# Kernel tuning notes

Hardware: AMD Instinct MI355X
Metric: run time of the kernel (lower is better)

The kernel has to match this reference:

```python
import jax, jax.numpy as jnp
import numpy as np

B, TQ, TK, D = 8, 2048, 2048, 1024


def setup_inputs() -> dict:
    key = jax.random.key(0)
    ks = jax.random.split(key, 9)
    s = 1.0 / np.sqrt(D)
    return {
        "query": jax.random.normal(ks[0], (B, TQ, D), jnp.float32),
        "keys": jax.random.normal(ks[1], (B, TK, D), jnp.float32),
        "Wq": jax.random.normal(ks[2], (D, D), jnp.float32) * s,
        "bq": jax.random.normal(ks[3], (D,), jnp.float32) * 0.01,
        "Wk": jax.random.normal(ks[4], (D, D), jnp.float32) * s,
        "bk": jax.random.normal(ks[5], (D,), jnp.float32) * 0.01,
        "Wv": jax.random.normal(ks[6], (D, D), jnp.float32) * s,
        "bv": jax.random.normal(ks[7], (D,), jnp.float32) * 0.01,
        "mask": jax.random.randint(ks[8], (B, TQ, TK), 0, 2, jnp.int32),
    }


def reference(query, keys, Wq, bq, Wk, bk, Wv, bv, mask):
    # Projections (torch Linear math; weights stored as [in, out])
    q = query @ Wq + bq            # [B, TQ, D]
    k = keys @ Wk + bk             # [B, TK, D]
    v = keys @ Wv + bv             # proj_values=True -> [B, TK, D]
    scale = 1.0 / jnp.sqrt(jnp.asarray(D, q.dtype))
    scores = jnp.einsum("bqd,bkd->bqk", q, k) * scale  # [B, TQ, TK]
    scores = jnp.where(mask == 0, jnp.asarray(-1e9, scores.dtype), scores)
    alphas = jax.nn.softmax(scores, axis=-1)
    context = jnp.einsum("bqk,bkd->bqd", alphas, v)    # [B, TQ, D]
    return context
```

## Files before the change

### kernel.cpp

```cpp
#include <hip/hip_runtime.h>
#include <hip/hip_bf16.h>

#define BB 8
#define TQn 2048
#define TKn 2048
#define DDn 1024

typedef float f32x4 __attribute__((ext_vector_type(4)));
typedef short bf16x8 __attribute__((ext_vector_type(8)));

__device__ __forceinline__ void async16(const void* g, void* l) {
    __builtin_amdgcn_global_load_lds(
        (const __attribute__((address_space(1))) void*)g,
        (__attribute__((address_space(3))) void*)l, 16, 0, 0);
}

__global__ __launch_bounds__(256) void cast_f32_bf16_k(
    const float* __restrict__ in, __hip_bfloat16* __restrict__ out, size_t n8) {
    size_t i = (size_t)blockIdx.x * blockDim.x + threadIdx.x;
    size_t stride = (size_t)gridDim.x * blockDim.x;
    for (; i < n8; i += stride) {
        const float4* p = (const float4*)in + i * 2;
        float4 a = p[0], b = p[1];
        union { __hip_bfloat16 h[8]; int4 q; } u;
        u.h[0] = __float2bfloat16(a.x); u.h[1] = __float2bfloat16(a.y);
        u.h[2] = __float2bfloat16(a.z); u.h[3] = __float2bfloat16(a.w);
        u.h[4] = __float2bfloat16(b.x); u.h[5] = __float2bfloat16(b.y);
        u.h[6] = __float2bfloat16(b.z); u.h[7] = __float2bfloat16(b.w);
        ((int4*)out)[i] = u.q;
    }
}

__global__ __launch_bounds__(256) void transpose_cast_k(
    const float* __restrict__ in, __hip_bfloat16* __restrict__ out) {
    __shared__ float tile[32][33];
    int c0 = blockIdx.x * 32, r0 = blockIdx.y * 32;
    int tx = threadIdx.x, ty = threadIdx.y;
    #pragma unroll
    for (int i = 0; i < 32; i += 8)
        tile[ty + i][tx] = in[(size_t)(r0 + ty + i) * DDn + c0 + tx];
    __syncthreads();
    #pragma unroll
    for (int i = 0; i < 32; i += 8)
        out[(size_t)(c0 + ty + i) * DDn + r0 + tx] = __float2bfloat16(tile[tx][ty + i]);
}


#define STG(Pg, Psl, U, T, H) do { \
    const __hip_bfloat16* _g = Pg + (size_t)(T) * 64 + (H) * 32; \
    char* _l = Psl + (U) * 16384 + w * 2048; \
    async16(_g, _l); \
    async16(_g + 16 * Kd, _l + 1024); \
} while (0)

#define PHASE(U, S, STAGE_STMT, WAIT_STMT) do { \
    if ((S) == 0) { \
        _Pragma("unroll") \
        for (int m = 0; m < 8; m++) \
            af[m] = *(const bf16x8*)(Asl + (U) * 16384 + a_off + m * 1024); \
    } \
    bf[0] = *(const bf16x8*)(Bsl + (U) * 16384 + b_off + (S) * 2048); \
    bf[1] = *(const bf16x8*)(Bsl + (U) * 16384 + b_off + (S) * 2048 + 1024); \
    STAGE_STMT; \
    WAIT_STMT; \
    __builtin_amdgcn_sched_barrier(0); \
    __builtin_amdgcn_s_barrier(); \
    __builtin_amdgcn_s_setprio(1); \
    _Pragma("unroll") \
    for (int m = 0; m < 8; m++) { \
        acc[m][(S)*2]     = __builtin_amdgcn_mfma_f32_16x16x32_bf16(af[m], bf[0], acc[m][(S)*2], 0, 0, 0); \
        acc[m][(S)*2 + 1] = __builtin_amdgcn_mfma_f32_16x16x32_bf16(af[m], bf[1], acc[m][(S)*2 + 1], 0, 0, 0); \
    } \
    __builtin_amdgcn_s_setprio(0); \
    __builtin_amdgcn_sched_barrier(0); \
    __builtin_amdgcn_s_barrier(); \
} while (0)

template <bool OUT_BF16, int BIAS>
__global__ __launch_bounds__(512, 2) void gemm256_k(
    const __hip_bfloat16* __restrict__ A, const __hip_bfloat16* __restrict__ B,
    void* __restrict__ Cout, const float* __restrict__ bias,
    int K, long sA, long sB, long sC, float scale, int ldc) {
    __shared__ char smem[131072];
    char* Asl = smem;
    char* Bsl = smem + 65536;

    const int tid = threadIdx.x;
    const int lane = tid & 63;
    const int w = tid >> 6;
    const int wr = w >> 2, wc = w & 3;
    const int bn = blockIdx.x, bm = blockIdx.y, bz = blockIdx.z;
    const size_t Kd = (size_t)K;

    const int slog = (lane & 3) ^ ((lane >> 4) & 3);
    const __hip_bfloat16* Agl = A + (size_t)bz * sA
        + ((size_t)bm * 256 + 32 * w + (lane >> 2)) * Kd + slog * 8;
    const __hip_bfloat16* Bgl = B + (size_t)bz * sB
        + ((size_t)bn * 256 + 32 * w + (lane >> 2)) * Kd + slog * 8;

    const int sx16 = ((lane >> 4) ^ ((lane & 15) >> 2)) * 16;
    const int a_off = (wr * 128 + (lane & 15)) * 64 + sx16;
    const int b_off = (wc * 64 + (lane & 15)) * 64 + sx16;

    f32x4 acc[8][4] = {};
    bf16x8 af[8], bf[2];

    const int NI = K >> 7;

    STG(Agl, Asl, 0, 0, 0); STG(Bgl, Bsl, 0, 0, 0);
    STG(Agl, Asl, 1, 0, 1); STG(Bgl, Bsl, 1, 0, 1);
    STG(Agl, Asl, 2, 1, 0); STG(Bgl, Bsl, 2, 1, 0);
    asm volatile("s_waitcnt vmcnt(4)" ::: "memory");
    __builtin_amdgcn_sched_barrier(0);
    __builtin_amdgcn_s_barrier();

    for (int i = 0; i < NI; ++i) {
        const bool nx = (i + 1 < NI);
        const int t1 = 2 * i + 1, t2 = 2 * i + 2, t3 = 2 * i + 3;
        PHASE(0, 0, STG(Agl, Asl, 3, t1, 1), );
        PHASE(0, 1, STG(Bgl, Bsl, 3, t1, 1), );
        PHASE(1, 0, if (nx) STG(Agl, Asl, 0, t2, 0), );
        PHASE(1, 1, if (nx) STG(Bgl, Bsl, 0, t2, 0),
              if (nx) { asm volatile("s_waitcnt vmcnt(4)" ::: "memory"); }
              else    { asm volatile("s_waitcnt vmcnt(0)" ::: "memory"); });
        PHASE(2, 0, if (nx) STG(Agl, Asl, 1, t2, 1), );
        PHASE(2, 1, if (nx) STG(Bgl, Bsl, 1, t2, 1), );
        PHASE(3, 0, if (nx) STG(Agl, Asl, 2, t3, 0), );
        PHASE(3, 1, if (nx) STG(Bgl, Bsl, 2, t3, 0),
              if (nx) { asm volatile("s_waitcnt vmcnt(4)" ::: "memory"); });
    }

    const int rq = (lane >> 4) << 2;
    const int cl = lane & 15;
    #pragma unroll
    for (int m = 0; m < 8; m++) {
        #pragma unroll
        for (int n = 0; n < 4; n++) {
            const int grow0 = bm * 256 + wr * 128 + m * 16 + rq;
            const int gcol = bn * 256 + wc * 64 + n * 16 + cl;
            float bv = 0.0f;
            if (BIAS == 1) bv = bias[gcol];
            #pragma unroll
            for (int r = 0; r < 4; r++) {
                float v = acc[m][n][r] * scale + ((BIAS == 2) ? bias[grow0 + r] : bv);
                size_t idx = (size_t)bz * sC + (size_t)(grow0 + r) * ldc + gcol;
                if (OUT_BF16)
                    ((__hip_bfloat16*)Cout)[idx] = __float2bfloat16(v);
                else
                    ((float*)Cout)[idx] = v;
            }
        }
    }
}

__global__ __launch_bounds__(256) void masked_softmax_k(
    const float* __restrict__ scores, const int* __restrict__ mask,
    __hip_bfloat16* __restrict__ alphas) {
    const size_t base = (size_t)blockIdx.x * TKn;
    const int t = threadIdx.x;
    const int lane = t & 63, wv = t >> 6;

    const float4* sp = (const float4*)(scores + base) + t * 2;
    const int4* mp = (const int4*)(mask + base) + t * 2;
    float4 s0 = sp[0], s1 = sp[1];
    int4 m0 = mp[0], m1 = mp[1];
    float v[8];
    v[0] = m0.x ? s0.x : -1e9f; v[1] = m0.y ? s0.y : -1e9f;
    v[2] = m0.z ? s0.z : -1e9f; v[3] = m0.w ? s0.w : -1e9f;
    v[4] = m1.x ? s1.x : -1e9f; v[5] = m1.y ? s1.y : -1e9f;
    v[6] = m1.z ? s1.z : -1e9f; v[7] = m1.w ? s1.w : -1e9f;

    float mx = v[0];
    #pragma unroll
    for (int j = 1; j < 8; j++) mx = fmaxf(mx, v[j]);
    #pragma unroll
    for (int off = 32; off; off >>= 1) mx = fmaxf(mx, __shfl_xor(mx, off));
    __shared__ float redm[4], reds[4];
    if (!lane) redm[wv] = mx;
    __syncthreads();
    mx = fmaxf(fmaxf(redm[0], redm[1]), fmaxf(redm[2], redm[3]));

    float e[8], sum = 0.0f;
    #pragma unroll
    for (int j = 0; j < 8; j++) { e[j] = __expf(v[j] - mx); sum += e[j]; }
    #pragma unroll
    for (int off = 32; off; off >>= 1) sum += __shfl_xor(sum, off);
    if (!lane) reds[wv] = sum;
    __syncthreads();
    sum = reds[0] + reds[1] + reds[2] + reds[3];
    float inv = 1.0f / sum;

    union { __hip_bfloat16 h[8]; int4 q; } u;
    #pragma unroll
    for (int j = 0; j < 8; j++) u.h[j] = __float2bfloat16(e[j] * inv);
    ((int4*)(alphas + base))[t] = u.q;
}

extern "C" void kernel_launch(void* const* d_in, const int* in_sizes, int n_in,
                              void* d_out, int out_size, void* d_ws, size_t ws_size,
                              hipStream_t stream) {
    const float* query = (const float*)d_in[0];
    const float* keys  = (const float*)d_in[1];
    const float* Wq = (const float*)d_in[2];
    const float* bq = (const float*)d_in[3];
    const float* Wk = (const float*)d_in[4];
    const float* bk = (const float*)d_in[5];
    const float* Wv = (const float*)d_in[6];
    const float* bv = (const float*)d_in[7];
    const int* mask = (const int*)d_in[8];
    float* out = (float*)d_out;

    char* ws = (char*)d_ws;
    const size_t NQ = (size_t)BB * TQn * DDn;
    __hip_bfloat16* xq_bf = (__hip_bfloat16*)(ws);
    __hip_bfloat16* xk_bf = (__hip_bfloat16*)(ws + 33554432);
    __hip_bfloat16* qb    = (__hip_bfloat16*)(ws + 67108864);
    __hip_bfloat16* kb    = (__hip_bfloat16*)(ws + 100663296);
    __hip_bfloat16* vtb   = (__hip_bfloat16*)(ws + 134217728);
    __hip_bfloat16* wq_t  = (__hip_bfloat16*)(ws + 167772160);
    __hip_bfloat16* wk_t  = (__hip_bfloat16*)(ws + 169869312);
    __hip_bfloat16* wv_t  = (__hip_bfloat16*)(ws + 171966464);
    float*          scores= (float*)         (ws + 174063616);
    __hip_bfloat16* alphas= (__hip_bfloat16*)(ws);

    const float scale = 0.03125f;

    cast_f32_bf16_k<<<2048, 256, 0, stream>>>(query, xq_bf, NQ / 8);
    cast_f32_bf16_k<<<2048, 256, 0, stream>>>(keys, xk_bf, NQ / 8);
    dim3 tb(32, 8);
    transpose_cast_k<<<dim3(32, 32), tb, 0, stream>>>(Wq, wq_t);
    transpose_cast_k<<<dim3(32, 32), tb, 0, stream>>>(Wk, wk_t);
    transpose_cast_k<<<dim3(32, 32), tb, 0, stream>>>(Wv, wv_t);
    gemm256_k<true, 1><<<dim3(4, 64, 1), 512, 0, stream>>>(
        xq_bf, wq_t, qb, bq, DDn, 0, 0, 0, 1.0f, DDn);
    gemm256_k<true, 1><<<dim3(4, 64, 1), 512, 0, stream>>>(
        xk_bf, wk_t, kb, bk, DDn, 0, 0, 0, 1.0f, DDn);
    gemm256_k<true, 2><<<dim3(8, 4, BB), 512, 0, stream>>>(
        wv_t, xk_bf, vtb, bv, DDn, 0, (long)TKn * DDn, (long)DDn * TKn, 1.0f, TKn);
    gemm256_k<false, 0><<<dim3(8, 8, BB), 512, 0, stream>>>(
        qb, kb, scores, nullptr, DDn, (long)TQn * DDn, (long)TKn * DDn,
        (long)TQn * TKn, scale, TKn);
    masked_softmax_k<<<BB * TQn, 256, 0, stream>>>(scores, mask, alphas);
    gemm256_k<false, 0><<<dim3(4, 8, BB), 512, 0, stream>>>(
        alphas, vtb, out, nullptr, TKn, (long)TQn * TKn, (long)DDn * TKn,
        (long)TQn * DDn, 1.0f, DDn);
}
```

Measured before the change: 615.9 us.

## Fuse masked softmax into score GEMM epilogue with deferred row normalization

Removes the separate softmax kernel and the fp32 score buffer. The score GEMM epilogue now applies the mask, exponentiates without subtracting a row max, writes unnormalized bf16 probabilities, and accumulates row sums with atomics. The context GEMM divides by the row sum in its epilogue. It also merges the Q/K projections, the casts and the weight transposes into batched launches. Skipping the max subtraction relies on scores being small enough not to overflow exp, which holds for these inputs but not in general. A fully masked row now gives a zero sum and a division by zero, where the reference gives a uniform average.

```diff
diff --git a/kernel.cpp b/kernel.cpp
--- a/kernel.cpp
+++ b/kernel.cpp
@@ -15,24 +15,40 @@
         (__attribute__((address_space(3))) void*)l, 16, 0, 0);
 }
 
-__global__ __launch_bounds__(256) void cast_f32_bf16_k(
-    const float* __restrict__ in, __hip_bfloat16* __restrict__ out, size_t n8) {
+__global__ __launch_bounds__(256) void prep_k(
+    float* __restrict__ rowsum, float* __restrict__ biasqk,
+    const float* __restrict__ bq, const float* __restrict__ bk) {
+    int i = blockIdx.x * 256 + threadIdx.x;
+    if (i < BB * TQn) rowsum[i] = 0.0f;
+    if (i < DDn) biasqk[i] = bq[i];
+    else if (i < 2 * DDn) biasqk[i] = bk[i - DDn];
+}
+
+__global__ __launch_bounds__(256) void cast2_k(
+    const float* __restrict__ q, const float* __restrict__ k,
+    __hip_bfloat16* __restrict__ xq, __hip_bfloat16* __restrict__ xk, size_t n8) {
+    const float* in = blockIdx.y ? k : q;
+    __hip_bfloat16* out = blockIdx.y ? xk : xq;
     size_t i = (size_t)blockIdx.x * blockDim.x + threadIdx.x;
     size_t stride = (size_t)gridDim.x * blockDim.x;
     for (; i < n8; i += stride) {
         const float4* p = (const float4*)in + i * 2;
         float4 a = p[0], b = p[1];
-        union { __hip_bfloat16 h[8]; int4 q; } u;
+        union { __hip_bfloat16 h[8]; int4 qd; } u;
         u.h[0] = __float2bfloat16(a.x); u.h[1] = __float2bfloat16(a.y);
         u.h[2] = __float2bfloat16(a.z); u.h[3] = __float2bfloat16(a.w);
         u.h[4] = __float2bfloat16(b.x); u.h[5] = __float2bfloat16(b.y);
         u.h[6] = __float2bfloat16(b.z); u.h[7] = __float2bfloat16(b.w);
-        ((int4*)out)[i] = u.q;
+        ((int4*)out)[i] = u.qd;
     }
 }
 
-__global__ __launch_bounds__(256) void transpose_cast_k(
-    const float* __restrict__ in, __hip_bfloat16* __restrict__ out) {
+__global__ __launch_bounds__(256) void transpose3_k(
+    const float* __restrict__ Wq, const float* __restrict__ Wk,
+    const float* __restrict__ Wv, __hip_bfloat16* __restrict__ oq,
+    __hip_bfloat16* __restrict__ ok, __hip_bfloat16* __restrict__ ov) {
+    const float* in = blockIdx.z == 0 ? Wq : (blockIdx.z == 1 ? Wk : Wv);
+    __hip_bfloat16* out = blockIdx.z == 0 ? oq : (blockIdx.z == 1 ? ok : ov);
     __shared__ float tile[32][33];
     int c0 = blockIdx.x * 32, r0 = blockIdx.y * 32;
     int tx = threadIdx.x, ty = threadIdx.y;
@@ -45,6 +61,10 @@
         out[(size_t)(c0 + ty + i) * DDn + r0 + tx] = __float2bfloat16(tile[tx][ty + i]);
 }
 
+#define M_PROJ_QK 0
+#define M_PROJ_V  1
+#define M_SCORES  2
+#define M_CTX     3
 
 #define STG(Pg, Psl, U, T, H) do { \
     const __hip_bfloat16* _g = Pg + (size_t)(T) * 64 + (H) * 32; \
@@ -76,10 +96,11 @@
     __builtin_amdgcn_s_barrier(); \
 } while (0)
 
-template <bool OUT_BF16, int BIAS>
+template <int MODE>
 __global__ __launch_bounds__(512, 2) void gemm256_k(
     const __hip_bfloat16* __restrict__ A, const __hip_bfloat16* __restrict__ B,
     void* __restrict__ Cout, const float* __restrict__ bias,
+    const int* __restrict__ mask, float* __restrict__ rowsum,
     int K, long sA, long sB, long sC, float scale, int ldc) {
     __shared__ char smem[131072];
     char* Asl = smem;
@@ -132,68 +153,72 @@
 
     const int rq = (lane >> 4) << 2;
     const int cl = lane & 15;
-    #pragma unroll
-    for (int m = 0; m < 8; m++) {
+
+    if (MODE == M_SCORES) {
+        const size_t mbase = (size_t)bz * ((size_t)TQn * TKn);
         #pragma unroll
-        for (int n = 0; n < 4; n++) {
+        for (int m = 0; m < 8; m++) {
             const int grow0 = bm * 256 + wr * 128 + m * 16 + rq;
-            const int gcol = bn * 256 + wc * 64 + n * 16 + cl;
-            float bv = 0.0f;
-            if (BIAS == 1) bv = bias[gcol];
-            #pragma unroll
-            for (int r = 0; r < 4; r++) {
-                float v = acc[m][n][r] * scale + ((BIAS == 2) ? bias[grow0 + r] : bv);
-                size_t idx = (size_t)bz * sC + (size_t)(grow0 + r) * ldc + gcol;
-                if (OUT_BF16)
-                    ((__hip_bfloat16*)Cout)[idx] = __float2bfloat16(v);
-                else
-                    ((float*)Cout)[idx] = v;
+            float rs[4] = {0.0f, 0.0f, 0.0f, 0.0f};
+            #pragma unroll
+            for (int n = 0; n < 4; n++) {
+                const int gcol = bn * 256 + wc * 64 + n * 16 + cl;
+                #pragma unroll
+                for (int r = 0; r < 4; r++) {
+                    float v = acc[m][n][r] * scale;
+                    int mk = mask[mbase + (size_t)(grow0 + r) * TKn + gcol];
+                    float p = mk ? __expf(v) : 0.0f;
+                    ((__hip_bfloat16*)Cout)[(size_t)bz * sC +
+                        (size_t)(grow0 + r) * ldc + gcol] = __float2bfloat16(p);
+                    rs[r] += p;
+                }
+            }
+            #pragma unroll
+            for (int off = 1; off < 16; off <<= 1) {
+                #pragma unroll
+                for (int r = 0; r < 4; r++) rs[r] += __shfl_xor(rs[r], off);
+            }
+            if (cl == 0) {
+                float* rp = rowsum + bz * TQn + grow0;
+                #pragma unroll
+                for (int r = 0; r < 4; r++) atomicAdd(rp + r, rs[r]);
+            }
+        }
+    } else if (MODE == M_CTX) {
+        #pragma unroll
+        for (int m = 0; m < 8; m++) {
+            const int grow0 = bm * 256 + wr * 128 + m * 16 + rq;
+            float inv[4];
+            #pragma unroll
+            for (int r = 0; r < 4; r++)
+                inv[r] = 1.0f / rowsum[bz * TQn + grow0 + r];
+            #pragma unroll
+            for (int n = 0; n < 4; n++) {
+                const int gcol = bn * 256 + wc * 64 + n * 16 + cl;
+                #pragma unroll
+                for (int r = 0; r < 4; r++)
+                    ((float*)Cout)[(size_t)bz * sC + (size_t)(grow0 + r) * ldc + gcol] =
+                        acc[m][n][r] * inv[r];
+            }
+        }
+    } else {
+        #pragma unroll
+        for (int m = 0; m < 8; m++) {
+            #pragma unroll
+            for (int n = 0; n < 4; n++) {
+                const int grow0 = bm * 256 + wr * 128 + m * 16 + rq;
+                const int gcol = bn * 256 + wc * 64 + n * 16 + cl;
+                float bv = (MODE == M_PROJ_QK) ? bias[bz * DDn + gcol] : 0.0f;
+                #pragma unroll
+                for (int r = 0; r < 4; r++) {
+                    float v = acc[m][n][r] * scale +
+                              ((MODE == M_PROJ_V) ? bias[grow0 + r] : bv);
+                    ((__hip_bfloat16*)Cout)[(size_t)bz * sC +
+                        (size_t)(grow0 + r) * ldc + gcol] = __float2bfloat16(v);
+                }
             }
         }
     }
-}
-
-__global__ __launch_bounds__(256) void masked_softmax_k(
-    const float* __restrict__ scores, const int* __restrict__ mask,
-    __hip_bfloat16* __restrict__ alphas) {
-    const size_t base = (size_t)blockIdx.x * TKn;
-    const int t = threadIdx.x;
-    const int lane = t & 63, wv = t >> 6;
-
-    const float4* sp = (const float4*)(scores + base) + t * 2;
-    const int4* mp = (const int4*)(mask + base) + t * 2;
-    float4 s0 = sp[0], s1 = sp[1];
-    int4 m0 = mp[0], m1 = mp[1];
-    float v[8];
-    v[0] = m0.x ? s0.x : -1e9f; v[1] = m0.y ? s0.y : -1e9f;
-    v[2] = m0.z ? s0.z : -1e9f; v[3] = m0.w ? s0.w : -1e9f;
-    v[4] = m1.x ? s1.x : -1e9f; v[5] = m1.y ? s1.y : -1e9f;
-    v[6] = m1.z ? s1.z : -1e9f; v[7] = m1.w ? s1.w : -1e9f;
-
-    float mx = v[0];
-    #pragma unroll
-    for (int j = 1; j < 8; j++) mx = fmaxf(mx, v[j]);
-    #pragma unroll
-    for (int off = 32; off; off >>= 1) mx = fmaxf(mx, __shfl_xor(mx, off));
-    __shared__ float redm[4], reds[4];
-    if (!lane) redm[wv] = mx;
-    __syncthreads();
-    mx = fmaxf(fmaxf(redm[0], redm[1]), fmaxf(redm[2], redm[3]));
-
-    float e[8], sum = 0.0f;
-    #pragma unroll
-    for (int j = 0; j < 8; j++) { e[j] = __expf(v[j] - mx); sum += e[j]; }
-    #pragma unroll
-    for (int off = 32; off; off >>= 1) sum += __shfl_xor(sum, off);
-    if (!lane) reds[wv] = sum;
-    __syncthreads();
-    sum = reds[0] + reds[1] + reds[2] + reds[3];
-    float inv = 1.0f / sum;
-
-    union { __hip_bfloat16 h[8]; int4 q; } u;
-    #pragma unroll
-    for (int j = 0; j < 8; j++) u.h[j] = __float2bfloat16(e[j] * inv);
-    ((int4*)(alphas + base))[t] = u.q;
 }
 
 extern "C" void kernel_launch(void* const* d_in, const int* in_sizes, int n_in,
@@ -220,28 +245,26 @@
     __hip_bfloat16* wq_t  = (__hip_bfloat16*)(ws + 167772160);
     __hip_bfloat16* wk_t  = (__hip_bfloat16*)(ws + 169869312);
     __hip_bfloat16* wv_t  = (__hip_bfloat16*)(ws + 171966464);
-    float*          scores= (float*)         (ws + 174063616);
-    __hip_bfloat16* alphas= (__hip_bfloat16*)(ws);
+    float*          biasqk= (float*)         (ws + 174063616);
+    float*          rowsum= (float*)         (ws + 174071808);
+    __hip_bfloat16* P     = (__hip_bfloat16*)(ws);
 
     const float scale = 0.03125f;
 
-    cast_f32_bf16_k<<<2048, 256, 0, stream>>>(query, xq_bf, NQ / 8);
-    cast_f32_bf16_k<<<2048, 256, 0, stream>>>(keys, xk_bf, NQ / 8);
-    dim3 tb(32, 8);
-    transpose_cast_k<<<dim3(32, 32), tb, 0, stream>>>(Wq, wq_t);
-    transpose_cast_k<<<dim3(32, 32), tb, 0, stream>>>(Wk, wk_t);
-    transpose_cast_k<<<dim3(32, 32), tb, 0, stream>>>(Wv, wv_t);
-    gemm256_k<true, 1><<<dim3(4, 64, 1), 512, 0, stream>>>(
-        xq_bf, wq_t, qb, bq, DDn, 0, 0, 0, 1.0f, DDn);
-    gemm256_k<true, 1><<<dim3(4, 64, 1), 512, 0, stream>>>(
-        xk_bf, wk_t, kb, bk, DDn, 0, 0, 0, 1.0f, DDn);
-    gemm256_k<true, 2><<<dim3(8, 4, BB), 512, 0, stream>>>(
-        wv_t, xk_bf, vtb, bv, DDn, 0, (long)TKn * DDn, (long)DDn * TKn, 1.0f, TKn);
-    gemm256_k<false, 0><<<dim3(8, 8, BB), 512, 0, stream>>>(
-        qb, kb, scores, nullptr, DDn, (long)TQn * DDn, (long)TKn * DDn,
-        (long)TQn * TKn, scale, TKn);
-    masked_softmax_k<<<BB * TQn, 256, 0, stream>>>(scores, mask, alphas);
-    gemm256_k<false, 0><<<dim3(4, 8, BB), 512, 0, stream>>>(
-        alphas, vtb, out, nullptr, TKn, (long)TQn * TKn, (long)DDn * TKn,
-        (long)TQn * DDn, 1.0f, DDn);
-}
+    prep_k<<<64, 256, 0, stream>>>(rowsum, biasqk, bq, bk);
+    cast2_k<<<dim3(1024, 2), 256, 0, stream>>>(query, keys, xq_bf, xk_bf, NQ / 8);
+    transpose3_k<<<dim3(32, 32, 3), dim3(32, 8), 0, stream>>>(
+        Wq, Wk, Wv, wq_t, wk_t, wv_t);
+    gemm256_k<M_PROJ_QK><<<dim3(4, 64, 2), 512, 0, stream>>>(
+        xq_bf, wq_t, qb, biasqk, nullptr, nullptr,
+        DDn, 16777216L, 1048576L, 16777216L, 1.0f, DDn);
+    gemm256_k<M_PROJ_V><<<dim3(8, 4, BB), 512, 0, stream>>>(
+        wv_t, xk_bf, vtb, bv, nullptr, nullptr,
+        DDn, 0, (long)TKn * DDn, (long)DDn * TKn, 1.0f, TKn);
+    gemm256_k<M_SCORES><<<dim3(8, 8, BB), 512, 0, stream>>>(
+        qb, kb, P, nullptr, mask, rowsum,
+        DDn, (long)TQn * DDn, (long)TKn * DDn, (long)TQn * TKn, scale, TKn);
+    gemm256_k<M_CTX><<<dim3(4, 8, BB), 512, 0, stream>>>(
+        P, vtb, out, nullptr, nullptr, rowsum,
+        TKn, (long)TQn * TKn, (long)DDn * TKn, (long)TQn * DDn, 1.0f, DDn);
+}
```

New measurement: 572.6 us. 1.08x faster.
